# Kernel tuning notes

Hardware: AMD Instinct MI355X
Metric: run time of the kernel (lower is better)

The kernel has to match this reference:

```python
import jax, jax.numpy as jnp
import numpy as np

IN_DIM = 4096
OUT_DIM = 4096
CODEBOOK_SIZE = 65536
LAYER_ID = 3
HASH_A, HASH_B, HASH_C = 10007, 20011, 40009
SIGN_HASH_A, SIGN_HASH_B, SIGN_HASH_C = 4099, 6151, 14887
SIGNED_HASH = True
BATCH = 8192


def _hash_tables():
    i = jnp.arange(OUT_DIM, dtype=jnp.int64 if jax.config.jax_enable_x64 else jnp.int32)[:, None]
    j = jnp.arange(IN_DIM, dtype=i.dtype)[None, :]
    idx = (i * HASH_A + j * HASH_B + LAYER_ID * HASH_C) % CODEBOOK_SIZE
    bits = (i * SIGN_HASH_A + j * SIGN_HASH_B + LAYER_ID * SIGN_HASH_C) % 2
    signs = bits.astype(jnp.float32) * 2.0 - 1.0
    return idx, signs


def setup_inputs() -> dict:
    key = jax.random.key(0)
    kx, kc = jax.random.split(key)
    x = jax.random.normal(kx, (BATCH, IN_DIM), dtype=jnp.float32)
    codebook = jax.random.normal(kc, (CODEBOOK_SIZE,), dtype=jnp.float32) * 0.01
    bias = jnp.zeros((OUT_DIM,), dtype=jnp.float32)
    return {"x": x, "codebook": codebook, "bias": bias}


def reference(x, codebook, bias):
    idx, signs = _hash_tables()  # [out_dim, in_dim] each
    weight = codebook[idx]  # gather from tiny codebook -> [out_dim, in_dim]
    if SIGNED_HASH:
        weight = weight * signs.astype(weight.dtype)
    # F.linear: y = x @ W^T + b
    return jnp.einsum('bi,oi->bo', x, weight) + bias
```

## Files before the change

kernel.cpp:

```cpp
#include <hip/hip_runtime.h>
#include <hip/hip_bf16.h>

constexpr int M_ = 8192;
constexpr int N_ = 4096;
constexpr int K_ = 4096;
constexpr int CBOOK = 65536;
constexpr int HA = 10007, HB = 20011;
constexpr int HC3 = 3 * 40009;

constexpr int BM = 256, BN = 256, BK = 32;
constexpr int NKT = K_ / BK;

using bf16x8 = __bf16 __attribute__((ext_vector_type(8)));
using f32x4  = float __attribute__((ext_vector_type(4)));
using u16x8  = unsigned short __attribute__((ext_vector_type(8)));

typedef __attribute__((address_space(3))) void lds_void_t;
typedef const __attribute__((address_space(1))) void gbl_void_t;

static __device__ __forceinline__ unsigned short f2bf(float f) {
    __bf16 h = (__bf16)f;
    return __builtin_bit_cast(unsigned short, h);
}

constexpr int GENB  = N_ * K_ / 8 / 256;
constexpr int CONVB = M_ * K_ / 8 / 256;

__global__ __launch_bounds__(256) void prep_kernel(const float* __restrict__ x,
                                                   const float* __restrict__ cb,
                                                   unsigned short* __restrict__ Wf,
                                                   unsigned short* __restrict__ xb) {
    const int b = blockIdx.x;
    if (b < GENB) {
        const int t    = b * 256 + threadIdx.x;
        const int slot = t & 1023;
        const int kt   = (t >> 10) & 127;
        const int nb   = t >> 17;
        const int row  = slot >> 2;
        const int key  = (row >> 1) & 3;
        const int n  = (nb << 8) + row;
        const int k0 = (kt << 5) + (((slot & 3) ^ key) << 3);
        const int h  = n * HA + k0 * HB + HC3;
        u16x8 out;
#pragma unroll
        for (int j = 0; j < 8; ++j) {
            const int idx = (h + j * HB) & (CBOOK - 1);
            float v = cb[idx];
            v = ((n ^ (k0 + j)) & 1) ? -v : v;
            out[j] = f2bf(v);
        }
        *reinterpret_cast<u16x8*>(&Wf[(size_t)t * 8]) = out;
    } else {
        const size_t t = (size_t)(b - GENB) * 256 + threadIdx.x;
        const float4* p = reinterpret_cast<const float4*>(x) + t * 2;
        const float4 a = p[0], c = p[1];
        u16x8 out;
        out[0] = f2bf(a.x); out[1] = f2bf(a.y); out[2] = f2bf(a.z); out[3] = f2bf(a.w);
        out[4] = f2bf(c.x); out[5] = f2bf(c.y); out[6] = f2bf(c.z); out[7] = f2bf(c.w);
        reinterpret_cast<u16x8*>(xb)[t] = out;
    }
}

__global__ __launch_bounds__(512, 2) void gemm_kernel(
        const unsigned short* __restrict__ A,
        const unsigned short* __restrict__ Wf,
        const float* __restrict__ bias,
        float* __restrict__ C) {
    __shared__ __align__(16) unsigned short sm[3 * 8192 * 2];
    unsigned short* As = sm;
    unsigned short* Bs = sm + 3 * 8192;

    const int tid  = threadIdx.x;
    const int lane = tid & 63;
    const int w    = tid >> 6;
    const int wm   = w >> 2;
    const int wn   = w & 3;
    const int m0 = blockIdx.y * BM;
    const int n0 = blockIdx.x * BN;

    const int quad = lane >> 4;
    const int l16  = lane & 15;

    const int sblk = (lane & 3) ^ ((lane >> 3) & 3);
    const unsigned short* aLane =
        A + (size_t)(m0 + w * 16 + (lane >> 2)) * K_ + sblk * 8;
    const unsigned short* bLane =
        Wf + (size_t)blockIdx.x * NKT * 8192 + tid * 8;

    const int rblk = (quad ^ ((l16 >> 1) & 3)) * 8;
    const unsigned short* aRd = As + (wm * 128 + l16) * 32 + rblk;
    const unsigned short* bRd = Bs + (wn * 64 + l16) * 32 + rblk;

    f32x4 acc[8][4] = {};

    auto STAGE = [&](int kt, int bs) {
#pragma unroll
        for (int r = 0; r < 2; ++r) {
            __builtin_amdgcn_global_load_lds(
                (gbl_void_t*)(aLane + (size_t)r * 128 * K_ + (size_t)kt * BK),
                (lds_void_t*)(As + bs * 8192 + (r * 512 + w * 64) * 8), 16, 0, 0);
            __builtin_amdgcn_global_load_lds(
                (gbl_void_t*)(bLane + (size_t)kt * 8192 + r * 4096),
                (lds_void_t*)(Bs + bs * 8192 + (r * 512 + w * 64) * 8), 16, 0, 0);
        }
    };

    STAGE(0, 0);
    STAGE(1, 1);

    int bC = 0;
    for (int kt = 0; kt < NKT; ++kt) {
        asm volatile("s_waitcnt lgkmcnt(0)" ::: "memory");
        if (kt < NKT - 1) asm volatile("s_waitcnt vmcnt(4)" ::: "memory");
        else              asm volatile("s_waitcnt vmcnt(0)" ::: "memory");
        __builtin_amdgcn_s_barrier();
        __builtin_amdgcn_sched_barrier(0);

        if (kt + 2 < NKT) {
            int bS = bC + 2; if (bS >= 3) bS -= 3;
            STAGE(kt + 2, bS);
        }

        bf16x8 bfr[4], afr[8];
#pragma unroll
        for (int nt = 0; nt < 4; ++nt)
            bfr[nt] = *reinterpret_cast<const bf16x8*>(bRd + bC * 8192 + nt * 512);
#pragma unroll
        for (int mt = 0; mt < 8; ++mt)
            afr[mt] = *reinterpret_cast<const bf16x8*>(aRd + bC * 8192 + mt * 512);

        __builtin_amdgcn_s_setprio(1);
#pragma unroll
        for (int mt = 0; mt < 8; ++mt)
#pragma unroll
            for (int nt = 0; nt < 4; ++nt)
                acc[mt][nt] = __builtin_amdgcn_mfma_f32_16x16x32_bf16(
                    afr[mt], bfr[nt], acc[mt][nt], 0, 0, 0);
        __builtin_amdgcn_s_setprio(0);

        ++bC; if (bC == 3) bC = 0;
    }

#pragma unroll
    for (int nt = 0; nt < 4; ++nt) {
        const int col = n0 + wn * 64 + nt * 16 + l16;
        const float bv = bias[col];
#pragma unroll
        for (int mt = 0; mt < 8; ++mt) {
            const int rowb = m0 + wm * 128 + mt * 16 + quad * 4;
#pragma unroll
            for (int r = 0; r < 4; ++r)
                C[(size_t)(rowb + r) * N_ + col] = acc[mt][nt][r] + bv;
        }
    }
}

__global__ __launch_bounds__(256) void naive_kernel(const float* __restrict__ x,
                                                    const float* __restrict__ cb,
                                                    const float* __restrict__ bias,
                                                    float* __restrict__ out) {
    const size_t t = (size_t)blockIdx.x * 256 + threadIdx.x;
    const int row = (int)(t / N_);
    const int col = (int)(t % N_);
    float s = bias[col];
    const float* xr = x + (size_t)row * K_;
    const int h = col * HA + HC3;
    for (int i = 0; i < K_; ++i) {
        float v = cb[(h + i * HB) & (CBOOK - 1)];
        s += xr[i] * (((col ^ i) & 1) ? -v : v);
    }
    out[t] = s;
}

extern "C" void kernel_launch(void* const* d_in, const int* in_sizes, int n_in,
                              void* d_out, int out_size, void* d_ws, size_t ws_size,
                              hipStream_t stream) {
    const float* x    = (const float*)d_in[0];
    const float* cb   = (const float*)d_in[1];
    const float* bias = (const float*)d_in[2];
    float* out = (float*)d_out;

    const size_t wBytes = (size_t)N_ * K_ * sizeof(unsigned short);
    const size_t xBytes = (size_t)M_ * K_ * sizeof(unsigned short);

    if (ws_size >= wBytes + xBytes) {
        unsigned short* Wf = (unsigned short*)d_ws;
        unsigned short* xb = (unsigned short*)((char*)d_ws + wBytes);
        prep_kernel<<<GENB + CONVB, 256, 0, stream>>>(x, cb, Wf, xb);
        gemm_kernel<<<dim3(N_ / BN, M_ / BM), 512, 0, stream>>>(xb, Wf, bias, out);
    } else {
        naive_kernel<<<(int)((size_t)M_ * N_ / 256), 256, 0, stream>>>(x, cb, bias, out);
    }
}
```

Before: 463.1 us.

## Precompute shifted signed codebook tables and split GEMM k-step into two halves

Exploits the hash structure: n*HA ≡ C0*n*HB (mod 65536), so each weight row is a contiguous slice of a sign-folded permuted codebook. A small pre-pass builds eight shifted bf16 copies so weight generation becomes a single aligned 16-byte load instead of eight scattered gathers. The GEMM main loop is also split into two half-steps, each issuing half of the next tile's global-to-LDS loads before its MFMA batch, with extra barriers. This adds a kernel launch and more barriers per k-step, and its correctness depends on the modular-inverse constant C0 being right.

```diff
diff --git a/kernel.cpp b/kernel.cpp
--- a/kernel.cpp
+++ b/kernel.cpp
@@ -8,6 +8,8 @@
 constexpr int HA = 10007, HB = 20011;
 constexpr int HC3 = 3 * 40009;
 
+constexpr int C0 = 197;
+
 constexpr int BM = 256, BN = 256, BK = 32;
 constexpr int NKT = K_ / BK;
 
@@ -23,13 +25,27 @@
     return __builtin_bit_cast(unsigned short, h);
 }
 
+constexpr int P2N   = 8 * 65536;
+constexpr int P2B   = P2N / 256;
+
+__global__ __launch_bounds__(256) void prep_p2(const float* __restrict__ cb,
+                                               unsigned short* __restrict__ P2p) {
+    const int t = blockIdx.x * 256 + threadIdx.x;
+    const int p = t >> 16;
+    const int i = t & 65535;
+    const int u = i + p;
+    float v = cb[(u * HB + HC3) & (CBOOK - 1)];
+    if (u & 1) v = -v;
+    P2p[t] = f2bf(v);
+}
+
 constexpr int GENB  = N_ * K_ / 8 / 256;
 constexpr int CONVB = M_ * K_ / 8 / 256;
 
-__global__ __launch_bounds__(256) void prep_kernel(const float* __restrict__ x,
-                                                   const float* __restrict__ cb,
-                                                   unsigned short* __restrict__ Wf,
-                                                   unsigned short* __restrict__ xb) {
+__global__ __launch_bounds__(256) void prep_main(const float* __restrict__ x,
+                                                 const unsigned short* __restrict__ P2p,
+                                                 unsigned short* __restrict__ Wf,
+                                                 unsigned short* __restrict__ xb) {
     const int b = blockIdx.x;
     if (b < GENB) {
         const int t    = b * 256 + threadIdx.x;
@@ -40,16 +56,10 @@
         const int key  = (row >> 1) & 3;
         const int n  = (nb << 8) + row;
         const int k0 = (kt << 5) + (((slot & 3) ^ key) << 3);
-        const int h  = n * HA + k0 * HB + HC3;
-        u16x8 out;
-#pragma unroll
-        for (int j = 0; j < 8; ++j) {
-            const int idx = (h + j * HB) & (CBOOK - 1);
-            float v = cb[idx];
-            v = ((n ^ (k0 + j)) & 1) ? -v : v;
-            out[j] = f2bf(v);
-        }
-        *reinterpret_cast<u16x8*>(&Wf[(size_t)t * 8]) = out;
+        const int u0 = (C0 * n + k0) & (CBOOK - 1);
+        const u16x8 w = *reinterpret_cast<const u16x8*>(
+            P2p + ((u0 & 7) << 16) + (u0 & 65528));
+        *reinterpret_cast<u16x8*>(&Wf[(size_t)t * 8]) = w;
     } else {
         const size_t t = (size_t)(b - GENB) * 256 + threadIdx.x;
         const float4* p = reinterpret_cast<const float4*>(x) + t * 2;
@@ -93,50 +103,75 @@
 
     f32x4 acc[8][4] = {};
 
-    auto STAGE = [&](int kt, int bs) {
-#pragma unroll
-        for (int r = 0; r < 2; ++r) {
-            __builtin_amdgcn_global_load_lds(
-                (gbl_void_t*)(aLane + (size_t)r * 128 * K_ + (size_t)kt * BK),
-                (lds_void_t*)(As + bs * 8192 + (r * 512 + w * 64) * 8), 16, 0, 0);
-            __builtin_amdgcn_global_load_lds(
-                (gbl_void_t*)(bLane + (size_t)kt * 8192 + r * 4096),
-                (lds_void_t*)(Bs + bs * 8192 + (r * 512 + w * 64) * 8), 16, 0, 0);
-        }
+    auto STAGE_HALF = [&](int kt, int bs, int r) {
+        __builtin_amdgcn_global_load_lds(
+            (gbl_void_t*)(aLane + (size_t)r * 128 * K_ + (size_t)kt * BK),
+            (lds_void_t*)(As + bs * 8192 + (r * 512 + w * 64) * 8), 16, 0, 0);
+        __builtin_amdgcn_global_load_lds(
+            (gbl_void_t*)(bLane + (size_t)kt * 8192 + r * 4096),
+            (lds_void_t*)(Bs + bs * 8192 + (r * 512 + w * 64) * 8), 16, 0, 0);
     };
 
-    STAGE(0, 0);
-    STAGE(1, 1);
+    STAGE_HALF(0, 0, 0); STAGE_HALF(0, 0, 1);
+    STAGE_HALF(1, 1, 0); STAGE_HALF(1, 1, 1);
+    asm volatile("s_waitcnt vmcnt(4)" ::: "memory");
+    __builtin_amdgcn_s_barrier();
+    __builtin_amdgcn_sched_barrier(0);
 
     int bC = 0;
     for (int kt = 0; kt < NKT; ++kt) {
-        asm volatile("s_waitcnt lgkmcnt(0)" ::: "memory");
-        if (kt < NKT - 1) asm volatile("s_waitcnt vmcnt(4)" ::: "memory");
-        else              asm volatile("s_waitcnt vmcnt(0)" ::: "memory");
-        __builtin_amdgcn_s_barrier();
-        __builtin_amdgcn_sched_barrier(0);
-
-        if (kt + 2 < NKT) {
-            int bS = bC + 2; if (bS >= 3) bS -= 3;
-            STAGE(kt + 2, bS);
-        }
-
-        bf16x8 bfr[4], afr[8];
+        int bS = bC + 2; if (bS >= 3) bS -= 3;
+        const bool st = (kt + 2 < NKT);
+
+        bf16x8 bfr[4], afr0[4];
 #pragma unroll
         for (int nt = 0; nt < 4; ++nt)
             bfr[nt] = *reinterpret_cast<const bf16x8*>(bRd + bC * 8192 + nt * 512);
 #pragma unroll
-        for (int mt = 0; mt < 8; ++mt)
-            afr[mt] = *reinterpret_cast<const bf16x8*>(aRd + bC * 8192 + mt * 512);
-
+        for (int mt = 0; mt < 4; ++mt)
+            afr0[mt] = *reinterpret_cast<const bf16x8*>(aRd + bC * 8192 + mt * 512);
+        if (st) STAGE_HALF(kt + 2, bS, 0);
+        __builtin_amdgcn_sched_barrier(0);
+        __builtin_amdgcn_s_barrier();
+        asm volatile("s_waitcnt lgkmcnt(0)" ::: "memory");
+        __builtin_amdgcn_sched_barrier(0);
         __builtin_amdgcn_s_setprio(1);
 #pragma unroll
-        for (int mt = 0; mt < 8; ++mt)
+        for (int mt = 0; mt < 4; ++mt)
 #pragma unroll
             for (int nt = 0; nt < 4; ++nt)
                 acc[mt][nt] = __builtin_amdgcn_mfma_f32_16x16x32_bf16(
-                    afr[mt], bfr[nt], acc[mt][nt], 0, 0, 0);
+                    afr0[mt], bfr[nt], acc[mt][nt], 0, 0, 0);
         __builtin_amdgcn_s_setprio(0);
+        __builtin_amdgcn_sched_barrier(0);
+        __builtin_amdgcn_s_barrier();
+        __builtin_amdgcn_sched_barrier(0);
+
+        bf16x8 afr1[4];
+#pragma unroll
+        for (int mt = 0; mt < 4; ++mt)
+            afr1[mt] = *reinterpret_cast<const bf16x8*>(aRd + bC * 8192 + (mt + 4) * 512);
+        if (st) STAGE_HALF(kt + 2, bS, 1);
+        __builtin_amdgcn_sched_barrier(0);
+        __builtin_amdgcn_s_barrier();
+        asm volatile("s_waitcnt lgkmcnt(0)" ::: "memory");
+        __builtin_amdgcn_sched_barrier(0);
+        __builtin_amdgcn_s_setprio(1);
+#pragma unroll
+        for (int mt = 0; mt < 4; ++mt)
+#pragma unroll
+            for (int nt = 0; nt < 4; ++nt)
+                acc[mt + 4][nt] = __builtin_amdgcn_mfma_f32_16x16x32_bf16(
+                    afr1[mt], bfr[nt], acc[mt + 4][nt], 0, 0, 0);
+        __builtin_amdgcn_s_setprio(0);
+        __builtin_amdgcn_sched_barrier(0);
+
+        if (kt < NKT - 1) {
+            if (st) asm volatile("s_waitcnt vmcnt(4)" ::: "memory");
+            else    asm volatile("s_waitcnt vmcnt(0)" ::: "memory");
+            __builtin_amdgcn_s_barrier();
+            __builtin_amdgcn_sched_barrier(0);
+        }
 
         ++bC; if (bC == 3) bC = 0;
     }
@@ -182,11 +217,14 @@
 
     const size_t wBytes = (size_t)N_ * K_ * sizeof(unsigned short);
     const size_t xBytes = (size_t)M_ * K_ * sizeof(unsigned short);
-
-    if (ws_size >= wBytes + xBytes) {
-        unsigned short* Wf = (unsigned short*)d_ws;
-        unsigned short* xb = (unsigned short*)((char*)d_ws + wBytes);
-        prep_kernel<<<GENB + CONVB, 256, 0, stream>>>(x, cb, Wf, xb);
+    const size_t pBytes = (size_t)P2N * sizeof(unsigned short);
+
+    if (ws_size >= wBytes + xBytes + pBytes) {
+        unsigned short* Wf  = (unsigned short*)d_ws;
+        unsigned short* xb  = (unsigned short*)((char*)d_ws + wBytes);
+        unsigned short* P2p = (unsigned short*)((char*)d_ws + wBytes + xBytes);
+        prep_p2<<<P2B, 256, 0, stream>>>(cb, P2p);
+        prep_main<<<GENB + CONVB, 256, 0, stream>>>(x, P2p, Wf, xb);
         gemm_kernel<<<dim3(N_ / BN, M_ / BM), 512, 0, stream>>>(xb, Wf, bias, out);
     } else {
         naive_kernel<<<(int)((size_t)M_ * N_ / 256), 256, 0, stream>>>(x, cb, bias, out);
```

Measured after the change: 451.8 us. 2.5% less time.
